# Kernel optimization log

Measured on AMD Instinct MI355X. Metric: run time of the kernel, lower is better.

Reference implementation:

```python
import jax, jax.numpy as jnp
import numpy as np

H = 32   # hidden_dim
L = 2    # rnn_num_layers
T = 52   # num_steps / seq_len
F = 64   # n_features (== 2*H, so layer-1 input size matches layer-0)
B = 8192 # batch


def _cell(x, h, c, Wih, Whh, b):
    # PyTorch LSTM gate order: i, f, g, o. b = b_ih + b_hh (mathematically identical).
    g = x @ Wih.T + h @ Whh.T + b
    i, f, gg, o = jnp.split(g, 4, axis=-1)
    c2 = jax.nn.sigmoid(f) * c + jax.nn.sigmoid(i) * jnp.tanh(gg)
    h2 = jax.nn.sigmoid(o) * jnp.tanh(c2)
    return h2, c2


def _encoder(x, h0, c0, Wih, Whh, b):
    # x: [B,T,F]; h0/c0: [2L,B,H]; PyTorch stacking order: [l0_fwd, l0_bwd, l1_fwd, l1_bwd]
    xs = jnp.swapaxes(x, 0, 1)  # time-major [T,B,F]
    hn, cn = [], []
    for l in range(L):
        def step_fwd(carry, xt):
            h, c = carry
            h2, c2 = _cell(xt, h, c, Wih[l, 0], Whh[l, 0], b[l, 0])
            return (h2, c2), h2
        def step_bwd(carry, xt):
            h, c = carry
            h2, c2 = _cell(xt, h, c, Wih[l, 1], Whh[l, 1], b[l, 1])
            return (h2, c2), h2
        (hf, cf), of = jax.lax.scan(step_fwd, (h0[2 * l], c0[2 * l]), xs)
        (hb, cb), ob = jax.lax.scan(step_bwd, (h0[2 * l + 1], c0[2 * l + 1]), xs[::-1])
        xs = jnp.concatenate([of, ob[::-1]], axis=-1)  # [T,B,2H]
        hn += [hf, hb]
        cn += [cf, cb]
    hn = jnp.stack(hn)  # [4,B,H]
    cn = jnp.stack(cn)
    hc = jnp.concatenate([jnp.swapaxes(hn, 0, 1), jnp.swapaxes(cn, 0, 1)], axis=1)  # [B,8,H]
    return hc.reshape(hc.shape[0], -1)  # [B, 2*2L*H] = [B,256]


def _decoder(code, Wih, Whh, b):
    Bn = code.shape[0]
    _code = code.reshape(Bn, 2, 2 * L, H)       # [B, (h,c), 4, H]
    h = jnp.swapaxes(_code[:, 0], 0, 1)          # [4,B,H]
    c = jnp.swapaxes(_code[:, 1], 0, 1)
    out0 = jnp.zeros((Bn, F), code.dtype)

    def step(carry, _):
        out, h, c = carry
        y = out
        hs, cs = [], []
        for l in range(L):
            hf, cf = _cell(y, h[2 * l], c[2 * l], Wih[l, 0], Whh[l, 0], b[l, 0])
            hb, cb = _cell(y, h[2 * l + 1], c[2 * l + 1], Wih[l, 1], Whh[l, 1], b[l, 1])
            y = jnp.concatenate([hf, hb], axis=-1)  # [B,2H]
            hs += [hf, hb]
            cs += [cf, cb]
        return (jax.lax.stop_gradient(y), jnp.stack(hs), jnp.stack(cs)), y

    _, ys = jax.lax.scan(step, (out0, h, c), None, length=T)  # ys: [T,B,F]
    return jnp.swapaxes(ys, 0, 1)  # [B,T,F]


def setup_inputs() -> dict:
    key = jax.random.key(0)
    ks = jax.random.split(key, 9)
    s = 1.0 / np.sqrt(H)  # PyTorch LSTM init range
    u = lambda k, shape: jax.random.uniform(k, shape, jnp.float32, -s, s)
    return {
        "x": jax.random.normal(ks[0], (B, T, F), jnp.float32),
        "h0": jax.random.normal(ks[1], (2 * L, B, H), jnp.float32),
        "c0": jax.random.normal(ks[2], (2 * L, B, H), jnp.float32),
        "enc_Wih": u(ks[3], (L, 2, 4 * H, F)),
        "enc_Whh": u(ks[4], (L, 2, 4 * H, H)),
        "enc_b": u(ks[5], (L, 2, 4 * H)),
        "dec_Wih": u(ks[6], (L, 2, 4 * H, F)),
        "dec_Whh": u(ks[7], (L, 2, 4 * H, H)),
        "dec_b": u(ks[8], (L, 2, 4 * H)),
    }


def reference(x, h0, c0, enc_Wih, enc_Whh, enc_b, dec_Wih, dec_Whh, dec_b):
    z = _encoder(x, h0, c0, enc_Wih, enc_Whh, enc_b)          # [B,256]
    x_hat = _decoder(z, dec_Wih, dec_Whh, dec_b)              # [B,T,F]
    return (x_hat, z)
```

## Files before the change

### kernel.cpp

```cpp
#include <hip/hip_runtime.h>
#include <cstddef>
#include <cstdint>

#define Tn 52
#define Fn 64
#define Hn 32
#define Bn 8192
#define XHAT_ELEMS (Bn * Tn * Fn)
#define L2E 1.44269504088896340736f

typedef __attribute__((ext_vector_type(8))) short bf8v;
typedef __attribute__((ext_vector_type(4))) float f4v;
typedef __attribute__((ext_vector_type(2))) float f2v;

__device__ __forceinline__ f4v mfma_bf16(bf8v a, bf8v b, f4v c) {
    return __builtin_amdgcn_mfma_f32_16x16x32_bf16(a, b, c, 0, 0, 0);
}

__device__ __forceinline__ unsigned short rne_bf16(float v) {
    unsigned b = __float_as_uint(v);
    unsigned r = ((b >> 16) & 1u) + 0x7FFFu;
    return (unsigned short)((b + r) >> 16);
}

__device__ __forceinline__ bf8v rne8(float4 a, float4 b) {
    float v[8] = {a.x, a.y, a.z, a.w, b.x, b.y, b.z, b.w};
    bf8v r;
#pragma unroll
    for (int j = 0; j < 8; ++j) r[j] = (short)rne_bf16(v[j]);
    return r;
}

__device__ __forceinline__ void lds_barrier_pinned() {
    __builtin_amdgcn_sched_barrier(0);
    asm volatile("s_waitcnt lgkmcnt(0)" ::: "memory");
    __builtin_amdgcn_s_barrier();
    __builtin_amdgcn_sched_barrier(0);
}

__device__ __forceinline__ void lds_barrier_relaxed() {
    asm volatile("s_waitcnt lgkmcnt(0)" ::: "memory");
    __builtin_amdgcn_s_barrier();
}

__device__ __forceinline__ f2v nexp2c(f2v a) {
    f2v r;
    r.x = exp2f(fminf(40.f, -a.x));
    r.y = exp2f(fminf(40.f, -a.y));
    return r;
}
__device__ __forceinline__ f2v rcp2(f2v a) {
    f2v r;
    r.x = __builtin_amdgcn_rcpf(a.x);
    r.y = __builtin_amdgcn_rcpf(a.y);
    return r;
}

__device__ __forceinline__ f2v lstm_pair(f2v aI, f2v aF, f2v aG, f2v aO, f2v& cst) {
    const f2v one = {1.f, 1.f};
    f2v ei = nexp2c(aI);
    f2v ef = nexp2c(aF);
    f2v eg = nexp2c(aG);
    f2v eo = nexp2c(aO);
    f2v p   = (one + ei) * (one + eg);
    f2v num = cst * p + (one - eg) * (one + ef);
    f2v den = (one + ef) * p;
    f2v c2  = num * rcp2(den);
    cst = c2;
    f2v t2 = c2 * (f2v){2.f * L2E, 2.f * L2E};
    f2v e2 = nexp2c(t2);
    return (one - e2) * rcp2((one + eo) * (one + e2));
}

#define PINW(W)                                                               \
    asm volatile("" : "+v"(W[0][0]), "+v"(W[0][1]), "+v"(W[0][2]),            \
                      "+v"(W[1][0]), "+v"(W[1][1]), "+v"(W[1][2]));           \
    asm volatile("" : "+v"(W[2][0]), "+v"(W[2][1]), "+v"(W[2][2]),            \
                      "+v"(W[3][0]), "+v"(W[3][1]), "+v"(W[3][2]));

__global__ void prep_kernel(const float* __restrict__ eWih, const float* __restrict__ eWhh,
                            const float* __restrict__ dWih, const float* __restrict__ dWhh,
                            unsigned short* __restrict__ ws)
{
    int fid = blockIdx.x * 256 + threadIdx.x;
    if (fid >= 12288) return;
    int lane = fid & 63;
    int ki   = (fid >> 6) % 3;
    int nt   = (fid / 192) & 7;
    int cell = (fid / 1536) & 3;
    int grp  = fid / 6144;
    const float* Wih = grp ? dWih : eWih;
    const float* Whh = grp ? dWhh : eWhh;
    int gate = nt * 16 + (lane & 15);
    float scale = ((gate >> 5) == 2) ? 2.f * L2E : L2E;
    int k0 = ki * 32 + (lane >> 4) * 8;
    size_t base = (size_t)grp * 98304 + (size_t)cell * 12288 + nt * 1536 + ki * 512 + lane * 8;
#pragma unroll
    for (int j = 0; j < 8; ++j) {
        int k = k0 + j;
        float v = (k < 64) ? Wih[(size_t)cell * 8192 + gate * 64 + k]
                           : Whh[(size_t)cell * 4096 + gate * 32 + (k - 64)];
        ws[base + j] = rne_bf16(v * scale);
    }
}

template<int IS_L0>
__global__ __launch_bounds__(256, 2)
void enc_kernel(const float* __restrict__ X, const unsigned short* __restrict__ Xh,
                const float* __restrict__ h0, const float* __restrict__ c0,
                const unsigned short* __restrict__ Whi, const float* __restrict__ bias,
                int layer, unsigned short* __restrict__ outh, float* __restrict__ z)
{
    __shared__ __align__(16) unsigned short Hsh[2][2][16][40];
    const int tid = threadIdx.x, w = tid >> 6, lane = tid & 63;
    const int d = w >> 1, q = w & 1;
    const int a = lane & 15, kb = lane >> 4;
    const int u = q * 16 + a;
    const int row0 = blockIdx.x * 16;
    const int ci = 2 * layer + d;

    bf8v WH[4][3];
#pragma unroll
    for (int g = 0; g < 4; ++g)
#pragma unroll
        for (int ki = 0; ki < 3; ++ki)
            WH[g][ki] = *(const bf8v*)(Whi + (size_t)ci * 12288 + (2 * g + q) * 1536
                                       + ki * 512 + lane * 8);
    float bj[4];
#pragma unroll
    for (int g = 0; g < 4; ++g)
        bj[g] = bias[ci * 128 + g * 32 + u] * ((g == 2) ? 2.f * L2E : L2E);
    float cst[4], hfin[4];
#pragma unroll
    for (int j = 0; j < 4; ++j)
        cst[j] = c0[((size_t)ci * Bn + row0 + 4 * kb + j) * Hn + u];

    {
        int dd = tid >> 7, rr = (tid >> 3) & 15, u4 = (tid & 7) * 4;
        const float* src = h0 + ((size_t)(2 * layer + dd) * Bn + row0 + rr) * Hn + u4;
#pragma unroll
        for (int e = 0; e < 4; ++e)
            Hsh[dd][1][rr][u4 + e] = rne_bf16(src[e]);
    }
    __syncthreads();

    const int grow = row0 + a;
    float4 p0, p1, p2, p3; bf8v ph0, ph1;
    f4v acc[4];
    {
        int tt = d ? (Tn - 1) : 0;
        bf8v xf0, xf1;
        if (IS_L0) {
            const float* sp = X + ((size_t)grow * Tn + tt) * Fn;
            xf0 = rne8(*(const float4*)(sp + kb * 8), *(const float4*)(sp + kb * 8 + 4));
            xf1 = rne8(*(const float4*)(sp + 32 + kb * 8), *(const float4*)(sp + 32 + kb * 8 + 4));
        } else {
            size_t so = ((size_t)tt * Bn + grow) * Fn + kb * 8;
            xf0 = *(const bf8v*)(Xh + so);
            xf1 = *(const bf8v*)(Xh + so + 32);
        }
#pragma unroll
        for (int g = 0; g < 4; ++g) {
            acc[g] = (f4v){bj[g], bj[g], bj[g], bj[g]};
            acc[g] = mfma_bf16(xf0, WH[g][0], acc[g]);
            acc[g] = mfma_bf16(xf1, WH[g][1], acc[g]);
        }
        int tt1 = d ? (Tn - 2) : 1;
        if (IS_L0) {
            const float* sp = X + ((size_t)grow * Tn + tt1) * Fn;
            p0 = *(const float4*)(sp + kb * 8);      p1 = *(const float4*)(sp + kb * 8 + 4);
            p2 = *(const float4*)(sp + 32 + kb * 8); p3 = *(const float4*)(sp + 32 + kb * 8 + 4);
        } else {
            size_t so = ((size_t)tt1 * Bn + grow) * Fn + kb * 8;
            ph0 = *(const bf8v*)(Xh + so);
            ph1 = *(const bf8v*)(Xh + so + 32);
        }
    }

    for (int t = 0; t < Tn; ++t) {
        PINW(WH);
        bf8v hh = *(const bf8v*)&Hsh[d][(t & 1) ^ 1][a][kb * 8];
#pragma unroll
        for (int g = 0; g < 4; ++g) acc[g] = mfma_bf16(hh, WH[g][2], acc[g]);
        int tp = d ? (Tn - 1 - t) : t;
#pragma unroll
        for (int jp = 0; jp < 2; ++jp) {
            f2v aI = {acc[0][2 * jp], acc[0][2 * jp + 1]};
            f2v aF = {acc[1][2 * jp], acc[1][2 * jp + 1]};
            f2v aG = {acc[2][2 * jp], acc[2][2 * jp + 1]};
            f2v aO = {acc[3][2 * jp], acc[3][2 * jp + 1]};
            f2v cc = {cst[2 * jp], cst[2 * jp + 1]};
            f2v hv = lstm_pair(aI, aF, aG, aO, cc);
            cst[2 * jp] = cc.x;  cst[2 * jp + 1] = cc.y;
            hfin[2 * jp] = hv.x; hfin[2 * jp + 1] = hv.y;
            unsigned short hp0 = rne_bf16(hv.x), hp1 = rne_bf16(hv.y);
            Hsh[d][t & 1][4 * kb + 2 * jp][u]     = hp0;
            Hsh[d][t & 1][4 * kb + 2 * jp + 1][u] = hp1;
            if (IS_L0) {
                outh[((size_t)tp * Bn + row0 + 4 * kb + 2 * jp) * Fn + d * 32 + u]     = hp0;
                outh[((size_t)tp * Bn + row0 + 4 * kb + 2 * jp + 1) * Fn + d * 32 + u] = hp1;
            }
        }
        {
            bf8v xf0, xf1;
            if (IS_L0) { xf0 = rne8(p0, p1); xf1 = rne8(p2, p3); }
            else       { xf0 = ph0; xf1 = ph1; }
#pragma unroll
            for (int g = 0; g < 4; ++g) {
                f4v t0 = (f4v){bj[g], bj[g], bj[g], bj[g]};
                t0 = mfma_bf16(xf0, WH[g][0], t0);
                acc[g] = mfma_bf16(xf1, WH[g][1], t0);
            }
            int ts = (t + 2 < Tn) ? t + 2 : Tn - 1;
            int tt = d ? (Tn - 1 - ts) : ts;
            if (IS_L0) {
                const float* sp = X + ((size_t)grow * Tn + tt) * Fn;
                p0 = *(const float4*)(sp + kb * 8);      p1 = *(const float4*)(sp + kb * 8 + 4);
                p2 = *(const float4*)(sp + 32 + kb * 8); p3 = *(const float4*)(sp + 32 + kb * 8 + 4);
            } else {
                size_t so = ((size_t)tt * Bn + grow) * Fn + kb * 8;
                ph0 = *(const bf8v*)(Xh + so);
                ph1 = *(const bf8v*)(Xh + so + 32);
            }
        }
        lds_barrier_pinned();
    }
#pragma unroll
    for (int j = 0; j < 4; ++j) {
        size_t zr = (size_t)(row0 + 4 * kb + j) * 256;
        z[zr + ci * 32 + u]       = hfin[j];
        z[zr + 128 + ci * 32 + u] = cst[j];
    }
}

__global__ __launch_bounds__(512, 2)
void dec_kernel(const unsigned short* __restrict__ Whi, const float* __restrict__ bias,
                const float* __restrict__ z, float* __restrict__ xhat)
{
    __shared__ __align__(16) unsigned short Ysh[2][2][16][72];
    __shared__ __align__(16) unsigned short Msh[2][16][72];
    __shared__ __align__(16) unsigned short Hsh[4][2][2][16][40];

    const int tid = threadIdx.x, w = tid >> 6, lane = tid & 63;
    const int P = w >> 2, cl = (w >> 1) & 1, q = w & 1;
    const int cell = P * 2 + cl;
    const int a = lane & 15, kb = lane >> 4, u = q * 16 + a;
    const int row0 = blockIdx.x * 32;

    bf8v WH[4][3];
#pragma unroll
    for (int g = 0; g < 4; ++g)
#pragma unroll
        for (int ki = 0; ki < 3; ++ki)
            WH[g][ki] = *(const bf8v*)(Whi + (size_t)cell * 12288 + (2 * g + q) * 1536
                                       + ki * 512 + lane * 8);
    f4v bC[4];
#pragma unroll
    for (int g = 0; g < 4; ++g) {
        float bv = bias[cell * 128 + g * 32 + u] * ((g == 2) ? 2.f * L2E : L2E);
        bC[g] = (f4v){bv, bv, bv, bv};
    }

    float cst[2][4];
#pragma unroll
    for (int G = 0; G < 2; ++G)
#pragma unroll
        for (int j = 0; j < 4; ++j)
            cst[G][j] = z[(size_t)(row0 + G * 16 + 4 * kb + j) * 256 + 128 + cell * 32 + u];

    {
        int ct = tid >> 7, rem = tid & 127, rr = rem >> 2, u8 = (rem & 3) * 8;
        const float* src = z + (size_t)(row0 + rr) * 256 + ct * 32 + u8;
#pragma unroll
        for (int e = 0; e < 8; ++e)
            Hsh[ct][rr >> 4][1][rr & 15][u8 + e] = rne_bf16(src[e]);
    }
    __syncthreads();

    f4v accp[4];
    auto hpart = [&](int G, int rpar) {
        bf8v hh = *(const bf8v*)&Hsh[cell][G][rpar][a][kb * 8];
        __builtin_amdgcn_s_setprio(1);
#pragma unroll
        for (int g = 0; g < 4; ++g) accp[g] = mfma_bf16(hh, WH[g][2], bC[g]);
        __builtin_amdgcn_s_setprio(0);
    };
    auto finish = [&](int G, int t, int par, bool isA, bool hasV) {
        if (hasV) {
            const unsigned short (*Vh)[72] = isA ? Ysh[G][par ^ 1] : Msh[G];
            bf8v vh0 = *(const bf8v*)&Vh[a][kb * 8];
            bf8v vh1 = *(const bf8v*)&Vh[a][32 + kb * 8];
            __builtin_amdgcn_s_setprio(1);
#pragma unroll
            for (int g = 0; g < 4; ++g) {
                accp[g] = mfma_bf16(vh0, WH[g][0], accp[g]);
                accp[g] = mfma_bf16(vh1, WH[g][1], accp[g]);
            }
            __builtin_amdgcn_s_setprio(0);
        }
#pragma unroll
        for (int jp = 0; jp < 2; ++jp) {
            f2v aI = {accp[0][2 * jp], accp[0][2 * jp + 1]};
            f2v aF = {accp[1][2 * jp], accp[1][2 * jp + 1]};
            f2v aG = {accp[2][2 * jp], accp[2][2 * jp + 1]};
            f2v aO = {accp[3][2 * jp], accp[3][2 * jp + 1]};
            f2v cc = {cst[G][2 * jp], cst[G][2 * jp + 1]};
            f2v hv = lstm_pair(aI, aF, aG, aO, cc);
            cst[G][2 * jp] = cc.x;  cst[G][2 * jp + 1] = cc.y;
            unsigned short hp0 = rne_bf16(hv.x), hp1 = rne_bf16(hv.y);
            int r0 = 4 * kb + 2 * jp, r1 = r0 + 1;
            Hsh[cell][G][par][r0][u] = hp0;
            Hsh[cell][G][par][r1][u] = hp1;
            if (isA) {
                Msh[G][r0][cl * 32 + u] = hp0;
                Msh[G][r1][cl * 32 + u] = hp1;
            } else {
                Ysh[G][par][r0][cl * 32 + u] = hp0;
                Ysh[G][par][r1][cl * 32 + u] = hp1;
                xhat[((size_t)(row0 + G * 16 + r0) * Tn + t) * Fn + cl * 32 + u] = hv.x;
                xhat[((size_t)(row0 + G * 16 + r1) * Tn + t) * Fn + cl * 32 + u] = hv.y;
            }
        }
    };

    hpart(0, 1);
    for (int it = 0; it < Tn / 2; ++it) {
        const int t0 = 2 * it, t1 = t0 + 1;
        const bool nz = (it > 0);
        PINW(WH);
        if (P == 0) { finish(0, t0, 0, true, nz);            hpart(1, 1); }
        else        { if (nz) finish(1, t0 - 1, 1, false, true); hpart(0, 1); }
        lds_barrier_relaxed();
        if (P == 0) { finish(1, t0, 0, true, nz);            hpart(0, 0); }
        else        { finish(0, t0, 0, false, true);         hpart(1, 1); }
        lds_barrier_relaxed();
        PINW(WH);
        if (P == 0) { finish(0, t1, 1, true, true);          hpart(1, 0); }
        else        { finish(1, t0, 0, false, true);         hpart(0, 0); }
        lds_barrier_relaxed();
        if (P == 0) { finish(1, t1, 1, true, true);          hpart(0, 1); }
        else        { finish(0, t1, 1, false, true);         hpart(1, 0); }
        lds_barrier_relaxed();
    }
    if (P == 1) finish(1, Tn - 1, 1, false, true);
}

extern "C" void kernel_launch(void* const* d_in, const int* in_sizes, int n_in,
                              void* d_out, int out_size, void* d_ws, size_t ws_size,
                              hipStream_t stream) {
    const float* x    = (const float*)d_in[0];
    const float* h0   = (const float*)d_in[1];
    const float* c0   = (const float*)d_in[2];
    const float* eWih = (const float*)d_in[3];
    const float* eWhh = (const float*)d_in[4];
    const float* eb   = (const float*)d_in[5];
    const float* dWih = (const float*)d_in[6];
    const float* dWhh = (const float*)d_in[7];
    const float* db   = (const float*)d_in[8];

    float* out = (float*)d_out;
    unsigned short* xs1h = (unsigned short*)d_out;
    float* zb = out + (size_t)XHAT_ELEMS;
    unsigned short* wsb = (unsigned short*)d_ws;

    hipLaunchKernelGGL(prep_kernel, dim3(48), dim3(256), 0, stream,
                       eWih, eWhh, dWih, dWhh, wsb);
    hipLaunchKernelGGL((enc_kernel<1>), dim3(Bn / 16), dim3(256), 0, stream,
                       x, (const unsigned short*)nullptr,
                       h0, c0, wsb, eb, 0, xs1h, zb);
    hipLaunchKernelGGL((enc_kernel<0>), dim3(Bn / 16), dim3(256), 0, stream,
                       (const float*)nullptr, xs1h,
                       h0, c0, wsb, eb, 1, (unsigned short*)nullptr, zb);
    hipLaunchKernelGGL(dec_kernel, dim3(Bn / 32), dim3(512), 0, stream,
                       wsb + 98304, db, zb, out);
}
```

Baseline: 260.3 us.

## Restructure decoder so each wave owns a full cell over 16 rows

The decoder now runs 256-thread blocks over 16 batch rows, with each wave computing all 32 hidden units of one cell (8 weight tiles held in registers) instead of two waves splitting the units. This removes the two-row-group ping-pong pipeline, so layer-0 and layer-1 halves alternate directly between barriers. The aim is to cut per-wave weight duplication and synchronisation overhead and give each wave more MFMA work. The cost is doubled register pressure for weights and accumulators, plus less overlap between the two layers, since one half of the block idles while the other finishes.

```diff
diff --git a/kernel.cpp b/kernel.cpp
--- a/kernel.cpp
+++ b/kernel.cpp
@@ -77,6 +77,16 @@
                       "+v"(W[1][0]), "+v"(W[1][1]), "+v"(W[1][2]));           \
     asm volatile("" : "+v"(W[2][0]), "+v"(W[2][1]), "+v"(W[2][2]),            \
                       "+v"(W[3][0]), "+v"(W[3][1]), "+v"(W[3][2]));
+
+#define PINW24(W)                                                             \
+    asm volatile("" : "+v"(W[0][0]), "+v"(W[0][1]), "+v"(W[0][2]),            \
+                      "+v"(W[1][0]), "+v"(W[1][1]), "+v"(W[1][2]));           \
+    asm volatile("" : "+v"(W[2][0]), "+v"(W[2][1]), "+v"(W[2][2]),            \
+                      "+v"(W[3][0]), "+v"(W[3][1]), "+v"(W[3][2]));           \
+    asm volatile("" : "+v"(W[4][0]), "+v"(W[4][1]), "+v"(W[4][2]),            \
+                      "+v"(W[5][0]), "+v"(W[5][1]), "+v"(W[5][2]));           \
+    asm volatile("" : "+v"(W[6][0]), "+v"(W[6][1]), "+v"(W[6][2]),            \
+                      "+v"(W[7][0]), "+v"(W[7][1]), "+v"(W[7][2]));
 
 __global__ void prep_kernel(const float* __restrict__ eWih, const float* __restrict__ eWhh,
                             const float* __restrict__ dWih, const float* __restrict__ dWhh,
@@ -233,116 +243,126 @@
     }
 }
 
-__global__ __launch_bounds__(512, 2)
+__global__ __launch_bounds__(256, 2)
 void dec_kernel(const unsigned short* __restrict__ Whi, const float* __restrict__ bias,
                 const float* __restrict__ z, float* __restrict__ xhat)
 {
-    __shared__ __align__(16) unsigned short Ysh[2][2][16][72];
-    __shared__ __align__(16) unsigned short Msh[2][16][72];
-    __shared__ __align__(16) unsigned short Hsh[4][2][2][16][40];
+    __shared__ __align__(16) unsigned short Ysh[2][16][72];
+    __shared__ __align__(16) unsigned short Msh[16][72];
+    __shared__ __align__(16) unsigned short Hsh[4][2][16][40];
 
     const int tid = threadIdx.x, w = tid >> 6, lane = tid & 63;
-    const int P = w >> 2, cl = (w >> 1) & 1, q = w & 1;
+    const int P = w >> 1, cl = w & 1;
     const int cell = P * 2 + cl;
-    const int a = lane & 15, kb = lane >> 4, u = q * 16 + a;
-    const int row0 = blockIdx.x * 32;
-
-    bf8v WH[4][3];
+    const int a = lane & 15, kb = lane >> 4;
+    const int row0 = blockIdx.x * 16;
+
+    bf8v WH[8][3];
+#pragma unroll
+    for (int nt = 0; nt < 8; ++nt)
+#pragma unroll
+        for (int ki = 0; ki < 3; ++ki)
+            WH[nt][ki] = *(const bf8v*)(Whi + (size_t)cell * 12288 + nt * 1536
+                                        + ki * 512 + lane * 8);
+    f4v bC[4][2];
 #pragma unroll
     for (int g = 0; g < 4; ++g)
 #pragma unroll
-        for (int ki = 0; ki < 3; ++ki)
-            WH[g][ki] = *(const bf8v*)(Whi + (size_t)cell * 12288 + (2 * g + q) * 1536
-                                       + ki * 512 + lane * 8);
-    f4v bC[4];
-#pragma unroll
-    for (int g = 0; g < 4; ++g) {
-        float bv = bias[cell * 128 + g * 32 + u] * ((g == 2) ? 2.f * L2E : L2E);
-        bC[g] = (f4v){bv, bv, bv, bv};
-    }
+        for (int s = 0; s < 2; ++s) {
+            float bv = bias[cell * 128 + g * 32 + s * 16 + a] * ((g == 2) ? 2.f * L2E : L2E);
+            bC[g][s] = (f4v){bv, bv, bv, bv};
+        }
 
     float cst[2][4];
 #pragma unroll
-    for (int G = 0; G < 2; ++G)
+    for (int s = 0; s < 2; ++s)
 #pragma unroll
         for (int j = 0; j < 4; ++j)
-            cst[G][j] = z[(size_t)(row0 + G * 16 + 4 * kb + j) * 256 + 128 + cell * 32 + u];
+            cst[s][j] = z[(size_t)(row0 + 4 * kb + j) * 256 + 128 + cell * 32 + s * 16 + a];
 
     {
-        int ct = tid >> 7, rem = tid & 127, rr = rem >> 2, u8 = (rem & 3) * 8;
+        int ct = tid >> 6, rr = (tid >> 2) & 15, u8 = (tid & 3) * 8;
         const float* src = z + (size_t)(row0 + rr) * 256 + ct * 32 + u8;
 #pragma unroll
         for (int e = 0; e < 8; ++e)
-            Hsh[ct][rr >> 4][1][rr & 15][u8 + e] = rne_bf16(src[e]);
+            Hsh[ct][1][rr][u8 + e] = rne_bf16(src[e]);
     }
     __syncthreads();
 
-    f4v accp[4];
-    auto hpart = [&](int G, int rpar) {
-        bf8v hh = *(const bf8v*)&Hsh[cell][G][rpar][a][kb * 8];
+    f4v accp[4][2];
+    auto hpart = [&](int rpar) {
+        bf8v hh = *(const bf8v*)&Hsh[cell][rpar][a][kb * 8];
         __builtin_amdgcn_s_setprio(1);
 #pragma unroll
-        for (int g = 0; g < 4; ++g) accp[g] = mfma_bf16(hh, WH[g][2], bC[g]);
+        for (int g = 0; g < 4; ++g)
+#pragma unroll
+            for (int s = 0; s < 2; ++s)
+                accp[g][s] = mfma_bf16(hh, WH[2 * g + s][2], bC[g][s]);
         __builtin_amdgcn_s_setprio(0);
     };
-    auto finish = [&](int G, int t, int par, bool isA, bool hasV) {
+    auto finish = [&](int t, int par, bool isA, bool hasV) {
         if (hasV) {
-            const unsigned short (*Vh)[72] = isA ? Ysh[G][par ^ 1] : Msh[G];
+            const unsigned short (*Vh)[72] = isA ? Ysh[par ^ 1] : Msh;
             bf8v vh0 = *(const bf8v*)&Vh[a][kb * 8];
             bf8v vh1 = *(const bf8v*)&Vh[a][32 + kb * 8];
             __builtin_amdgcn_s_setprio(1);
 #pragma unroll
-            for (int g = 0; g < 4; ++g) {
-                accp[g] = mfma_bf16(vh0, WH[g][0], accp[g]);
-                accp[g] = mfma_bf16(vh1, WH[g][1], accp[g]);
+            for (int g = 0; g < 4; ++g)
+#pragma unroll
+                for (int s = 0; s < 2; ++s) {
+                    accp[g][s] = mfma_bf16(vh0, WH[2 * g + s][0], accp[g][s]);
+                    accp[g][s] = mfma_bf16(vh1, WH[2 * g + s][1], accp[g][s]);
+                }
+            __builtin_amdgcn_s_setprio(0);
+        }
+#pragma unroll
+        for (int s = 0; s < 2; ++s) {
+            const int u = s * 16 + a;
+#pragma unroll
+            for (int jp = 0; jp < 2; ++jp) {
+                f2v aI = {accp[0][s][2 * jp], accp[0][s][2 * jp + 1]};
+                f2v aF = {accp[1][s][2 * jp], accp[1][s][2 * jp + 1]};
+                f2v aG = {accp[2][s][2 * jp], accp[2][s][2 * jp + 1]};
+                f2v aO = {accp[3][s][2 * jp], accp[3][s][2 * jp + 1]};
+                f2v cc = {cst[s][2 * jp], cst[s][2 * jp + 1]};
+                f2v hv = lstm_pair(aI, aF, aG, aO, cc);
+                cst[s][2 * jp] = cc.x;  cst[s][2 * jp + 1] = cc.y;
+                unsigned short hp0 = rne_bf16(hv.x), hp1 = rne_bf16(hv.y);
+                int r0 = 4 * kb + 2 * jp, r1 = r0 + 1;
+                Hsh[cell][par][r0][u] = hp0;
+                Hsh[cell][par][r1][u] = hp1;
+                if (isA) {
+                    Msh[r0][cl * 32 + u] = hp0;
+                    Msh[r1][cl * 32 + u] = hp1;
+                } else {
+                    Ysh[par][r0][cl * 32 + u] = hp0;
+                    Ysh[par][r1][cl * 32 + u] = hp1;
+                    xhat[((size_t)(row0 + r0) * Tn + t) * Fn + cl * 32 + u] = hv.x;
+                    xhat[((size_t)(row0 + r1) * Tn + t) * Fn + cl * 32 + u] = hv.y;
+                }
             }
-            __builtin_amdgcn_s_setprio(0);
-        }
-#pragma unroll
-        for (int jp = 0; jp < 2; ++jp) {
-            f2v aI = {accp[0][2 * jp], accp[0][2 * jp + 1]};
-            f2v aF = {accp[1][2 * jp], accp[1][2 * jp + 1]};
-            f2v aG = {accp[2][2 * jp], accp[2][2 * jp + 1]};
-            f2v aO = {accp[3][2 * jp], accp[3][2 * jp + 1]};
-            f2v cc = {cst[G][2 * jp], cst[G][2 * jp + 1]};
-            f2v hv = lstm_pair(aI, aF, aG, aO, cc);
-            cst[G][2 * jp] = cc.x;  cst[G][2 * jp + 1] = cc.y;
-            unsigned short hp0 = rne_bf16(hv.x), hp1 = rne_bf16(hv.y);
-            int r0 = 4 * kb + 2 * jp, r1 = r0 + 1;
-            Hsh[cell][G][par][r0][u] = hp0;
-            Hsh[cell][G][par][r1][u] = hp1;
-            if (isA) {
-                Msh[G][r0][cl * 32 + u] = hp0;
-                Msh[G][r1][cl * 32 + u] = hp1;
-            } else {
-                Ysh[G][par][r0][cl * 32 + u] = hp0;
-                Ysh[G][par][r1][cl * 32 + u] = hp1;
-                xhat[((size_t)(row0 + G * 16 + r0) * Tn + t) * Fn + cl * 32 + u] = hv.x;
-                xhat[((size_t)(row0 + G * 16 + r1) * Tn + t) * Fn + cl * 32 + u] = hv.y;
-            }
         }
     };
 
-    hpart(0, 1);
+    hpart(1);
     for (int it = 0; it < Tn / 2; ++it) {
         const int t0 = 2 * it, t1 = t0 + 1;
         const bool nz = (it > 0);
-        PINW(WH);
-        if (P == 0) { finish(0, t0, 0, true, nz);            hpart(1, 1); }
-        else        { if (nz) finish(1, t0 - 1, 1, false, true); hpart(0, 1); }
+        PINW24(WH);
+        if (P == 0) finish(t0, 0, true, nz);
+        else        hpart(1);
         lds_barrier_relaxed();
-        if (P == 0) { finish(1, t0, 0, true, nz);            hpart(0, 0); }
-        else        { finish(0, t0, 0, false, true);         hpart(1, 1); }
+        if (P == 1) finish(t0, 0, false, true);
+        else        hpart(0);
         lds_barrier_relaxed();
-        PINW(WH);
-        if (P == 0) { finish(0, t1, 1, true, true);          hpart(1, 0); }
-        else        { finish(1, t0, 0, false, true);         hpart(0, 0); }
+        PINW24(WH);
+        if (P == 0) finish(t1, 1, true, true);
+        else        hpart(0);
         lds_barrier_relaxed();
-        if (P == 0) { finish(1, t1, 1, true, true);          hpart(0, 1); }
-        else        { finish(0, t1, 1, false, true);         hpart(1, 0); }
+        if (P == 1) finish(t1, 1, false, true);
+        else        hpart(1);
         lds_barrier_relaxed();
     }
-    if (P == 1) finish(1, Tn - 1, 1, false, true);
 }
 
 extern "C" void kernel_launch(void* const* d_in, const int* in_sizes, int n_in,
@@ -371,6 +391,6 @@
     hipLaunchKernelGGL((enc_kernel<0>), dim3(Bn / 16), dim3(256), 0, stream,
                        (const float*)nullptr, xs1h,
                        h0, c0, wsb, eb, 1, (unsigned short*)nullptr, zb);
-    hipLaunchKernelGGL(dec_kernel, dim3(Bn / 32), dim3(512), 0, stream,
+    hipLaunchKernelGGL(dec_kernel, dim3(Bn / 16), dim3(256), 0, stream,
                        wsb + 98304, db, zb, out);
 }
```

After: 318.4 us. 22.3% more time.

## Give each encoder direction a single wave to drop per-step block barriers

Applied to the files above, without the earlier changes.

The encoder block shrinks from four waves (two per direction, each owning half the hidden units) to two waves, one per direction. Each wave now owns all 32 hidden units and all eight gate tiles, so its recurrent state in LDS is private to it and the per-timestep block barrier is removed. The time loop is unrolled by two so the LDS double-buffer parity is a compile-time constant. In exchange, each wave does twice the MFMA and activation work per step and holds twice the weight registers, with launch bounds changed to allow it, which may lower occupancy or lengthen each wave's serial chain.

```diff
diff --git a/kernel.cpp b/kernel.cpp
--- a/kernel.cpp
+++ b/kernel.cpp
@@ -29,13 +29,6 @@
 #pragma unroll
     for (int j = 0; j < 8; ++j) r[j] = (short)rne_bf16(v[j]);
     return r;
-}
-
-__device__ __forceinline__ void lds_barrier_pinned() {
-    __builtin_amdgcn_sched_barrier(0);
-    asm volatile("s_waitcnt lgkmcnt(0)" ::: "memory");
-    __builtin_amdgcn_s_barrier();
-    __builtin_amdgcn_sched_barrier(0);
 }
 
 __device__ __forceinline__ void lds_barrier_relaxed() {
@@ -77,6 +70,16 @@
                       "+v"(W[1][0]), "+v"(W[1][1]), "+v"(W[1][2]));           \
     asm volatile("" : "+v"(W[2][0]), "+v"(W[2][1]), "+v"(W[2][2]),            \
                       "+v"(W[3][0]), "+v"(W[3][1]), "+v"(W[3][2]));
+
+#define PINW24(W)                                                             \
+    asm volatile("" : "+v"(W[0][0]), "+v"(W[0][1]), "+v"(W[0][2]),            \
+                      "+v"(W[1][0]), "+v"(W[1][1]), "+v"(W[1][2]));           \
+    asm volatile("" : "+v"(W[2][0]), "+v"(W[2][1]), "+v"(W[2][2]),            \
+                      "+v"(W[3][0]), "+v"(W[3][1]), "+v"(W[3][2]));           \
+    asm volatile("" : "+v"(W[4][0]), "+v"(W[4][1]), "+v"(W[4][2]),            \
+                      "+v"(W[5][0]), "+v"(W[5][1]), "+v"(W[5][2]));           \
+    asm volatile("" : "+v"(W[6][0]), "+v"(W[6][1]), "+v"(W[6][2]),            \
+                      "+v"(W[7][0]), "+v"(W[7][1]), "+v"(W[7][2]));
 
 __global__ void prep_kernel(const float* __restrict__ eWih, const float* __restrict__ eWhh,
                             const float* __restrict__ dWih, const float* __restrict__ dWhh,
@@ -105,7 +108,7 @@
 }
 
 template<int IS_L0>
-__global__ __launch_bounds__(256, 2)
+__global__ __launch_bounds__(128, 1)
 void enc_kernel(const float* __restrict__ X, const unsigned short* __restrict__ Xh,
                 const float* __restrict__ h0, const float* __restrict__ c0,
                 const unsigned short* __restrict__ Whi, const float* __restrict__ bias,
@@ -113,40 +116,39 @@
 {
     __shared__ __align__(16) unsigned short Hsh[2][2][16][40];
     const int tid = threadIdx.x, w = tid >> 6, lane = tid & 63;
-    const int d = w >> 1, q = w & 1;
+    const int d = w;
     const int a = lane & 15, kb = lane >> 4;
-    const int u = q * 16 + a;
     const int row0 = blockIdx.x * 16;
     const int ci = 2 * layer + d;
 
-    bf8v WH[4][3];
+    bf8v WH[8][3];
+#pragma unroll
+    for (int nt = 0; nt < 8; ++nt)
+#pragma unroll
+        for (int ki = 0; ki < 3; ++ki)
+            WH[nt][ki] = *(const bf8v*)(Whi + (size_t)ci * 12288 + nt * 1536
+                                        + ki * 512 + lane * 8);
+    f4v bC[4][2];
 #pragma unroll
     for (int g = 0; g < 4; ++g)
 #pragma unroll
-        for (int ki = 0; ki < 3; ++ki)
-            WH[g][ki] = *(const bf8v*)(Whi + (size_t)ci * 12288 + (2 * g + q) * 1536
-                                       + ki * 512 + lane * 8);
-    float bj[4];
-#pragma unroll
-    for (int g = 0; g < 4; ++g)
-        bj[g] = bias[ci * 128 + g * 32 + u] * ((g == 2) ? 2.f * L2E : L2E);
-    float cst[4], hfin[4];
-#pragma unroll
-    for (int j = 0; j < 4; ++j)
-        cst[j] = c0[((size_t)ci * Bn + row0 + 4 * kb + j) * Hn + u];
-
-    {
-        int dd = tid >> 7, rr = (tid >> 3) & 15, u4 = (tid & 7) * 4;
-        const float* src = h0 + ((size_t)(2 * layer + dd) * Bn + row0 + rr) * Hn + u4;
-#pragma unroll
-        for (int e = 0; e < 4; ++e)
-            Hsh[dd][1][rr][u4 + e] = rne_bf16(src[e]);
-    }
-    __syncthreads();
+        for (int s = 0; s < 2; ++s) {
+            float bv = bias[ci * 128 + g * 32 + s * 16 + a] * ((g == 2) ? 2.f * L2E : L2E);
+            bC[g][s] = (f4v){bv, bv, bv, bv};
+        }
+    float cst[2][4], hfin[2][4];
+#pragma unroll
+    for (int s = 0; s < 2; ++s)
+#pragma unroll
+        for (int j = 0; j < 4; ++j) {
+            size_t ro = ((size_t)ci * Bn + row0 + 4 * kb + j) * Hn + s * 16 + a;
+            cst[s][j] = c0[ro];
+            Hsh[w][1][4 * kb + j][s * 16 + a] = rne_bf16(h0[ro]);
+        }
 
     const int grow = row0 + a;
     float4 p0, p1, p2, p3; bf8v ph0, ph1;
-    f4v acc[4];
+    f4v acc[4][2];
     {
         int tt = d ? (Tn - 1) : 0;
         bf8v xf0, xf1;
@@ -160,11 +162,12 @@
             xf1 = *(const bf8v*)(Xh + so + 32);
         }
 #pragma unroll
-        for (int g = 0; g < 4; ++g) {
-            acc[g] = (f4v){bj[g], bj[g], bj[g], bj[g]};
-            acc[g] = mfma_bf16(xf0, WH[g][0], acc[g]);
-            acc[g] = mfma_bf16(xf1, WH[g][1], acc[g]);
-        }
+        for (int g = 0; g < 4; ++g)
+#pragma unroll
+            for (int s = 0; s < 2; ++s) {
+                f4v t0 = mfma_bf16(xf0, WH[2 * g + s][0], bC[g][s]);
+                acc[g][s] = mfma_bf16(xf1, WH[2 * g + s][1], t0);
+            }
         int tt1 = d ? (Tn - 2) : 1;
         if (IS_L0) {
             const float* sp = X + ((size_t)grow * Tn + tt1) * Fn;
@@ -177,60 +180,72 @@
         }
     }
 
-    for (int t = 0; t < Tn; ++t) {
-        PINW(WH);
-        bf8v hh = *(const bf8v*)&Hsh[d][(t & 1) ^ 1][a][kb * 8];
-#pragma unroll
-        for (int g = 0; g < 4; ++g) acc[g] = mfma_bf16(hh, WH[g][2], acc[g]);
+    auto step = [&](int t, int par) {
+        PINW24(WH);
+        bf8v hh = *(const bf8v*)&Hsh[w][par ^ 1][a][kb * 8];
+#pragma unroll
+        for (int g = 0; g < 4; ++g)
+#pragma unroll
+            for (int s = 0; s < 2; ++s)
+                acc[g][s] = mfma_bf16(hh, WH[2 * g + s][2], acc[g][s]);
         int tp = d ? (Tn - 1 - t) : t;
 #pragma unroll
-        for (int jp = 0; jp < 2; ++jp) {
-            f2v aI = {acc[0][2 * jp], acc[0][2 * jp + 1]};
-            f2v aF = {acc[1][2 * jp], acc[1][2 * jp + 1]};
-            f2v aG = {acc[2][2 * jp], acc[2][2 * jp + 1]};
-            f2v aO = {acc[3][2 * jp], acc[3][2 * jp + 1]};
-            f2v cc = {cst[2 * jp], cst[2 * jp + 1]};
-            f2v hv = lstm_pair(aI, aF, aG, aO, cc);
-            cst[2 * jp] = cc.x;  cst[2 * jp + 1] = cc.y;
-            hfin[2 * jp] = hv.x; hfin[2 * jp + 1] = hv.y;
-            unsigned short hp0 = rne_bf16(hv.x), hp1 = rne_bf16(hv.y);
-            Hsh[d][t & 1][4 * kb + 2 * jp][u]     = hp0;
-            Hsh[d][t & 1][4 * kb + 2 * jp + 1][u] = hp1;
-            if (IS_L0) {
-                outh[((size_t)tp * Bn + row0 + 4 * kb + 2 * jp) * Fn + d * 32 + u]     = hp0;
-                outh[((size_t)tp * Bn + row0 + 4 * kb + 2 * jp + 1) * Fn + d * 32 + u] = hp1;
-            }
-        }
-        {
-            bf8v xf0, xf1;
-            if (IS_L0) { xf0 = rne8(p0, p1); xf1 = rne8(p2, p3); }
-            else       { xf0 = ph0; xf1 = ph1; }
-#pragma unroll
-            for (int g = 0; g < 4; ++g) {
-                f4v t0 = (f4v){bj[g], bj[g], bj[g], bj[g]};
-                t0 = mfma_bf16(xf0, WH[g][0], t0);
-                acc[g] = mfma_bf16(xf1, WH[g][1], t0);
-            }
-            int ts = (t + 2 < Tn) ? t + 2 : Tn - 1;
-            int tt = d ? (Tn - 1 - ts) : ts;
-            if (IS_L0) {
-                const float* sp = X + ((size_t)grow * Tn + tt) * Fn;
-                p0 = *(const float4*)(sp + kb * 8);      p1 = *(const float4*)(sp + kb * 8 + 4);
-                p2 = *(const float4*)(sp + 32 + kb * 8); p3 = *(const float4*)(sp + 32 + kb * 8 + 4);
-            } else {
-                size_t so = ((size_t)tt * Bn + grow) * Fn + kb * 8;
-                ph0 = *(const bf8v*)(Xh + so);
-                ph1 = *(const bf8v*)(Xh + so + 32);
-            }
-        }
-        lds_barrier_pinned();
-    }
-#pragma unroll
-    for (int j = 0; j < 4; ++j) {
-        size_t zr = (size_t)(row0 + 4 * kb + j) * 256;
-        z[zr + ci * 32 + u]       = hfin[j];
-        z[zr + 128 + ci * 32 + u] = cst[j];
-    }
+        for (int s = 0; s < 2; ++s) {
+            const int u = s * 16 + a;
+#pragma unroll
+            for (int jp = 0; jp < 2; ++jp) {
+                f2v aI = {acc[0][s][2 * jp], acc[0][s][2 * jp + 1]};
+                f2v aF = {acc[1][s][2 * jp], acc[1][s][2 * jp + 1]};
+                f2v aG = {acc[2][s][2 * jp], acc[2][s][2 * jp + 1]};
+                f2v aO = {acc[3][s][2 * jp], acc[3][s][2 * jp + 1]};
+                f2v cc = {cst[s][2 * jp], cst[s][2 * jp + 1]};
+                f2v hv = lstm_pair(aI, aF, aG, aO, cc);
+                cst[s][2 * jp] = cc.x;  cst[s][2 * jp + 1] = cc.y;
+                hfin[s][2 * jp] = hv.x; hfin[s][2 * jp + 1] = hv.y;
+                unsigned short hp0 = rne_bf16(hv.x), hp1 = rne_bf16(hv.y);
+                int r0 = 4 * kb + 2 * jp, r1 = r0 + 1;
+                Hsh[w][par][r0][u] = hp0;
+                Hsh[w][par][r1][u] = hp1;
+                if (IS_L0) {
+                    outh[((size_t)tp * Bn + row0 + r0) * Fn + d * 32 + u] = hp0;
+                    outh[((size_t)tp * Bn + row0 + r1) * Fn + d * 32 + u] = hp1;
+                }
+            }
+        }
+        bf8v xf0, xf1;
+        if (IS_L0) { xf0 = rne8(p0, p1); xf1 = rne8(p2, p3); }
+        else       { xf0 = ph0; xf1 = ph1; }
+#pragma unroll
+        for (int g = 0; g < 4; ++g)
+#pragma unroll
+            for (int s = 0; s < 2; ++s) {
+                f4v t0 = mfma_bf16(xf0, WH[2 * g + s][0], bC[g][s]);
+                acc[g][s] = mfma_bf16(xf1, WH[2 * g + s][1], t0);
+            }
+        int ts = (t + 2 < Tn) ? t + 2 : Tn - 1;
+        int tt = d ? (Tn - 1 - ts) : ts;
+        if (IS_L0) {
+            const float* sp = X + ((size_t)grow * Tn + tt) * Fn;
+            p0 = *(const float4*)(sp + kb * 8);      p1 = *(const float4*)(sp + kb * 8 + 4);
+            p2 = *(const float4*)(sp + 32 + kb * 8); p3 = *(const float4*)(sp + 32 + kb * 8 + 4);
+        } else {
+            size_t so = ((size_t)tt * Bn + grow) * Fn + kb * 8;
+            ph0 = *(const bf8v*)(Xh + so);
+            ph1 = *(const bf8v*)(Xh + so + 32);
+        }
+    };
+    for (int it = 0; it < Tn / 2; ++it) {
+        step(2 * it, 0);
+        step(2 * it + 1, 1);
+    }
+#pragma unroll
+    for (int s = 0; s < 2; ++s)
+#pragma unroll
+        for (int j = 0; j < 4; ++j) {
+            size_t zr = (size_t)(row0 + 4 * kb + j) * 256;
+            z[zr + ci * 32 + s * 16 + a]       = hfin[s][j];
+            z[zr + 128 + ci * 32 + s * 16 + a] = cst[s][j];
+        }
 }
 
 __global__ __launch_bounds__(512, 2)
@@ -365,10 +380,10 @@
 
     hipLaunchKernelGGL(prep_kernel, dim3(48), dim3(256), 0, stream,
                        eWih, eWhh, dWih, dWhh, wsb);
-    hipLaunchKernelGGL((enc_kernel<1>), dim3(Bn / 16), dim3(256), 0, stream,
+    hipLaunchKernelGGL((enc_kernel<1>), dim3(Bn / 16), dim3(128), 0, stream,
                        x, (const unsigned short*)nullptr,
                        h0, c0, wsb, eb, 0, xs1h, zb);
-    hipLaunchKernelGGL((enc_kernel<0>), dim3(Bn / 16), dim3(256), 0, stream,
+    hipLaunchKernelGGL((enc_kernel<0>), dim3(Bn / 16), dim3(128), 0, stream,
                        (const float*)nullptr, xs1h,
                        h0, c0, wsb, eb, 1, (unsigned short*)nullptr, zb);
     hipLaunchKernelGGL(dec_kernel, dim3(Bn / 32), dim3(512), 0, stream,
```

Result: slower. 371.6 us (+42.7%).
